# Kernel tuning notes

Hardware: AMD Instinct MI355X
Metric: run time of the kernel (lower is better)

The kernel has to match this reference:

```python
import jax, jax.numpy as jnp
import numpy as np

B, T, C = 8, 2048, 1024


def setup_inputs() -> dict:
    key = jax.random.key(0)
    ks = jax.random.split(key, 7)
    s = 0.02  # typical init scale for weights
    return {
        "x": jax.random.normal(ks[0], (B, T, C), jnp.float32),
        "wq": jax.random.normal(ks[1], (C, C), jnp.float32) * s,
        "bq": jax.random.normal(ks[2], (C,), jnp.float32) * s,
        "wk": jax.random.normal(ks[3], (C, C), jnp.float32) * s,
        "bk": jax.random.normal(ks[4], (C,), jnp.float32) * s,
        "wv": jax.random.normal(ks[5], (C, C), jnp.float32) * s,
        "bv": jax.random.normal(ks[6], (C,), jnp.float32) * s,
    }


def reference(x, wq, bq, wk, bk, wv, bv):
    # x: [B, T, C]; torch Linear stores weight as [out, in] -> x @ W.T + b
    Bx, Tx, Cx = x.shape
    Q = x @ wq.T + bq  # [B, T, C]
    K = x @ wk.T + bk
    V = x @ wv.T + bv
    # NOTE: source computes K @ Q^T (keys index rows, queries index columns)
    scores = jnp.einsum("btc,bsc->bts", K, Q) / jnp.sqrt(jnp.float32(Cx))  # [B, T, T]
    causal = jnp.tril(jnp.ones((Tx, Tx), dtype=bool))  # mask==0 above diagonal
    scores = jnp.where(causal, scores, -jnp.inf)
    # torch masked_fill with a (1,1,T,T) mask broadcasts scores to (1,B,T,T)
    scores = scores[None]  # [1, B, T, T]
    w = jax.nn.softmax(scores, axis=-1)
    out = jnp.einsum("abts,bsc->abtc", w, V)  # [1, B, T, C]
    return out
```

## Files before the change

kernel.cpp:

```cpp
#include <hip/hip_runtime.h>
#include <stdint.h>

typedef unsigned short u16;
typedef __attribute__((ext_vector_type(8))) __bf16 bf16x8;
typedef __attribute__((ext_vector_type(4))) float f32x4;

#define DEVI __device__ __forceinline__

DEVI u16 f32_to_bf16(float f) {
  uint32_t u = __builtin_bit_cast(uint32_t, f);
  u += 0x7FFFu + ((u >> 16) & 1u);
  return (u16)(u >> 16);
}

DEVI void gl2lds16(const void* g, void* l) {
  __builtin_amdgcn_global_load_lds(
      (const __attribute__((address_space(1))) void*)g,
      (__attribute__((address_space(3))) void*)l, 16, 0, 0);
}

#define S_BATCH 2228224

__global__ void cast_all_kernel(const float* __restrict__ x,
                                const float* __restrict__ wq,
                                const float* __restrict__ wk,
                                const float* __restrict__ wv,
                                u16* __restrict__ xb, u16* __restrict__ wb,
                                float* __restrict__ sums) {
  const int i0 = blockIdx.x * blockDim.x + threadIdx.x;
  const int stride = gridDim.x * blockDim.x;
  for (int j = i0; j < 4194304; j += stride) {
    const float4 v = ((const float4*)x)[j];
    ushort4 o;
    o.x = f32_to_bf16(v.x);
    o.y = f32_to_bf16(v.y);
    o.z = f32_to_bf16(v.z);
    o.w = f32_to_bf16(v.w);
    ((ushort4*)xb)[j] = o;
  }
  for (int j = i0; j < 786432; j += stride) {
    const int z = j >> 18;
    const int r = j & 262143;
    const float* src = (z == 0) ? wq : (z == 1) ? wk : wv;
    const float4 v = ((const float4*)src)[r];
    ushort4 o;
    o.x = f32_to_bf16(v.x);
    o.y = f32_to_bf16(v.y);
    o.z = f32_to_bf16(v.z);
    o.w = f32_to_bf16(v.w);
    ((ushort4*)(wb + (size_t)z * 1048576))[r] = o;
  }
  if (i0 < 4096) ((float4*)sums)[i0] = (float4){0.f, 0.f, 0.f, 0.f};
}

__global__ __launch_bounds__(512, 2) void qkv_kernel(
    const u16* __restrict__ xb, const u16* __restrict__ wb,
    const float* __restrict__ bq, const float* __restrict__ bk,
    const float* __restrict__ bv, u16* __restrict__ Qb, u16* __restrict__ Kb,
    u16* __restrict__ Vt) {
  __shared__ __align__(16) u16 lds[65536];

  const int id = blockIdx.x;
  const int wg = (id & 7) * 96 + (id >> 3);
  const int g = wg >> 3, u = wg & 7;
  const int z = g >> 5;
  const int tp = g & 31;
  const int tmt = tp * 2 + (u >> 2);
  const int tct = u & 3;

  int m0, n0;
  const u16* Aptr;
  const u16* Bptr;
  if (z < 2) {
    m0 = tct * 256;
    n0 = tmt * 256;
    Aptr = wb + (size_t)z * 1048576 + (size_t)m0 * 1024;
    Bptr = xb + (size_t)n0 * 1024;
  } else {
    m0 = tmt * 256;
    n0 = tct * 256;
    Aptr = xb + (size_t)m0 * 1024;
    Bptr = wb + (size_t)2 * 1048576 + (size_t)n0 * 1024;
  }

  const int tid = threadIdx.x;
  const int srow = tid >> 3;
  const int sgrp = ((tid & 7) - srow) & 7;
  const u16* Ag = Aptr + (size_t)srow * 1024 + sgrp * 8;
  const u16* Bg = Bptr + (size_t)srow * 1024 + sgrp * 8;
  char* ldsDst = (char*)lds + tid * 16;

#define ST_A0(kt) do { const u16* s_ = Ag + (kt) * 64;           char* d_ = ldsDst + (((kt) & 1) * 65536);         gl2lds16(s_, d_); gl2lds16(s_ + 65536, d_ + 8192); } while (0)
#define ST_A1(kt) do { const u16* s_ = Ag + 131072 + (kt) * 64;  char* d_ = ldsDst + (((kt) & 1) * 65536) + 16384; gl2lds16(s_, d_); gl2lds16(s_ + 65536, d_ + 8192); } while (0)
#define ST_B0(kt) do { const u16* s_ = Bg + (kt) * 64;           char* d_ = ldsDst + (((kt) & 1) * 65536) + 32768; gl2lds16(s_, d_); gl2lds16(s_ + 65536, d_ + 8192); } while (0)
#define ST_B1(kt) do { const u16* s_ = Bg + 131072 + (kt) * 64;  char* d_ = ldsDst + (((kt) & 1) * 65536) + 49152; gl2lds16(s_, d_); gl2lds16(s_ + 65536, d_ + 8192); } while (0)

  ST_A0(0); ST_B0(0); ST_B1(0); ST_A1(0);
  ST_A0(1); ST_B0(1); ST_B1(1);

  const int lane = tid & 63, wid = tid >> 6;
  const int wr = wid >> 2, wc = wid & 3;
  const int l15 = lane & 15, quad = lane >> 4;

  int aoff[4][2], boff[2][2];
#pragma unroll
  for (int i_ = 0; i_ < 4; ++i_) {
    const int arow = wr * 64 + i_ * 16 + l15;
#pragma unroll
    for (int k_ = 0; k_ < 2; ++k_)
      aoff[i_][k_] = arow * 64 + ((k_ * 4 + quad + arow) & 7) * 8;
  }
#pragma unroll
  for (int j_ = 0; j_ < 2; ++j_) {
    const int brow = wc * 32 + j_ * 16 + l15;
#pragma unroll
    for (int k_ = 0; k_ < 2; ++k_)
      boff[j_][k_] = brow * 64 + ((k_ * 4 + quad + brow) & 7) * 8;
  }

  f32x4 acc[2][2][4][2];
#pragma unroll
  for (int a_ = 0; a_ < 2; ++a_)
#pragma unroll
    for (int b_ = 0; b_ < 2; ++b_)
#pragma unroll
      for (int i_ = 0; i_ < 4; ++i_)
#pragma unroll
        for (int j_ = 0; j_ < 2; ++j_)
          acc[a_][b_][i_][j_] = (f32x4){0.f, 0.f, 0.f, 0.f};

  bf16x8 af[4][2], bfr[2][2][2];

#define LOADA(qm, buf) do { const u16* p_ = lds + (buf) * 32768 + (qm) * 8192; \
  _Pragma("unroll") for (int i_ = 0; i_ < 4; ++i_) \
  _Pragma("unroll") for (int k_ = 0; k_ < 2; ++k_) \
    af[i_][k_] = *(const bf16x8*)(p_ + aoff[i_][k_]); } while (0)
#define LOADB(qn, buf) do { const u16* p_ = lds + (buf) * 32768 + 16384 + (qn) * 8192; \
  _Pragma("unroll") for (int j_ = 0; j_ < 2; ++j_) \
  _Pragma("unroll") for (int k_ = 0; k_ < 2; ++k_) \
    bfr[qn][j_][k_] = *(const bf16x8*)(p_ + boff[j_][k_]); } while (0)
#define MMA(qm, qn) do { \
  _Pragma("unroll") for (int i_ = 0; i_ < 4; ++i_) \
  _Pragma("unroll") for (int j_ = 0; j_ < 2; ++j_) \
  _Pragma("unroll") for (int k_ = 0; k_ < 2; ++k_) \
    acc[qm][qn][i_][j_] = __builtin_amdgcn_mfma_f32_16x16x32_bf16( \
        af[i_][k_], bfr[qn][j_][k_], acc[qm][qn][i_][j_], 0, 0, 0); } while (0)

#define BAR __builtin_amdgcn_s_barrier()
#define WLG0 asm volatile("s_waitcnt lgkmcnt(0)")
#define WLG8 asm volatile("s_waitcnt lgkmcnt(8)")
#define PRIO1 __builtin_amdgcn_s_setprio(1)
#define PRIO0 __builtin_amdgcn_s_setprio(0)
#define WVM6 asm volatile("s_waitcnt vmcnt(6)" ::: "memory")
#define WVM0 asm volatile("s_waitcnt vmcnt(0)" ::: "memory")

  WVM6;
  BAR;

#pragma unroll 1
  for (int it = 0; it < 7; ++it) {
    const int j0 = 2 * it;
    LOADA(0, 0); LOADB(0, 0); ST_A1(j0 + 1); WLG8;
    BAR; WLG0; PRIO1; MMA(0, 0); PRIO0; BAR;
    LOADB(1, 0); ST_A0(j0 + 2);
    BAR; WLG0; PRIO1; MMA(0, 1); PRIO0; BAR;
    LOADA(1, 0); ST_B0(j0 + 2);
    BAR; WLG0; PRIO1; MMA(1, 1); PRIO0; BAR;
    ST_B1(j0 + 2);
    BAR; PRIO1; MMA(1, 0); PRIO0;
    WVM6;
    BAR;
    LOADA(0, 1); LOADB(0, 1); ST_A1(j0 + 2); WLG8;
    BAR; WLG0; PRIO1; MMA(0, 0); PRIO0; BAR;
    LOADB(1, 1); ST_A0(j0 + 3);
    BAR; WLG0; PRIO1; MMA(0, 1); PRIO0; BAR;
    LOADA(1, 1); ST_B0(j0 + 3);
    BAR; WLG0; PRIO1; MMA(1, 1); PRIO0; BAR;
    ST_B1(j0 + 3);
    BAR; PRIO1; MMA(1, 0); PRIO0;
    WVM6;
    BAR;
  }
  {
    LOADA(0, 0); LOADB(0, 0); ST_A1(15); WLG8;
    BAR; WLG0; PRIO1; MMA(0, 0); PRIO0; BAR;
    LOADB(1, 0);
    BAR; WLG0; PRIO1; MMA(0, 1); PRIO0; BAR;
    LOADA(1, 0);
    BAR; WLG0; PRIO1; MMA(1, 1); PRIO0; BAR;
    BAR; PRIO1; MMA(1, 0); PRIO0;
    WVM0;
    BAR;
    LOADA(0, 1); LOADB(0, 1); WLG8;
    BAR; WLG0; PRIO1; MMA(0, 0); PRIO0; BAR;
    LOADB(1, 1);
    BAR; WLG0; PRIO1; MMA(0, 1); PRIO0; BAR;
    LOADA(1, 1);
    BAR; WLG0; PRIO1; MMA(1, 1); PRIO0; BAR;
    PRIO1; MMA(1, 0); PRIO0;
    BAR;
  }

  if (z < 2) {
    const float* bias = (z == 0) ? bq : bk;
    u16* Out = (z == 0) ? Qb : Kb;
#pragma unroll
    for (int th = 0; th < 2; ++th) {
      if (th) __syncthreads();
#pragma unroll
      for (int qm = 0; qm < 2; ++qm)
#pragma unroll
        for (int i_ = 0; i_ < 4; ++i_) {
          const int c = qm * 128 + wr * 64 + i_ * 16 + quad * 4;
          const float4 b4 = *(const float4*)(bias + m0 + c);
#pragma unroll
          for (int j_ = 0; j_ < 2; ++j_) {
            const int row = wc * 32 + j_ * 16 + l15;
            ushort4 o;
            o.x = f32_to_bf16(acc[qm][th][i_][j_][0] + b4.x);
            o.y = f32_to_bf16(acc[qm][th][i_][j_][1] + b4.y);
            o.z = f32_to_bf16(acc[qm][th][i_][j_][2] + b4.z);
            o.w = f32_to_bf16(acc[qm][th][i_][j_][3] + b4.w);
            *(ushort4*)(lds + row * 264 + c) = o;
          }
        }
      __syncthreads();
#pragma unroll
      for (int p = 0; p < 8; ++p) {
        const int row = p * 16 + (tid >> 5);
        const int c0 = (tid & 31) * 8;
        const uint4 v = *(const uint4*)(lds + row * 264 + c0);
        *(uint4*)(Out + (size_t)(n0 + th * 128 + row) * 1024 + m0 + c0) = v;
      }
    }
  } else {
    const int b = m0 >> 11;
    const int t0b = m0 & 2047;
    u16* Out = Vt + (size_t)b * 2097152;
#pragma unroll
    for (int th = 0; th < 2; ++th) {
      if (th) __syncthreads();
#pragma unroll
      for (int j_ = 0; j_ < 2; ++j_) {
        const int row = wc * 32 + j_ * 16 + l15;
        const float bb = bv[n0 + th * 128 + row];
#pragma unroll
        for (int qm = 0; qm < 2; ++qm)
#pragma unroll
          for (int i_ = 0; i_ < 4; ++i_) {
            const int c = qm * 128 + wr * 64 + i_ * 16 + quad * 4;
            ushort4 o;
            o.x = f32_to_bf16(acc[qm][th][i_][j_][0] + bb);
            o.y = f32_to_bf16(acc[qm][th][i_][j_][1] + bb);
            o.z = f32_to_bf16(acc[qm][th][i_][j_][2] + bb);
            o.w = f32_to_bf16(acc[qm][th][i_][j_][3] + bb);
            *(ushort4*)(lds + row * 264 + c) = o;
          }
      }
      __syncthreads();
#pragma unroll
      for (int p = 0; p < 8; ++p) {
        const int row = p * 16 + (tid >> 5);
        const int c0 = (tid & 31) * 8;
        const uint4 v = *(const uint4*)(lds + row * 264 + c0);
        *(uint4*)(Out + (size_t)(n0 + th * 128 + row) * 2048 + t0b + c0) = v;
      }
    }
  }
#undef ST_A0
#undef ST_A1
#undef ST_B0
#undef ST_B1
#undef LOADA
#undef LOADB
#undef MMA
#undef BAR
#undef WLG0
#undef WLG8
#undef PRIO1
#undef PRIO0
#undef WVM6
#undef WVM0
}

__global__ __launch_bounds__(512, 2) void score_kernel(const u16* __restrict__ Kb,
                                                       const u16* __restrict__ Qb,
                                                       u16* __restrict__ Spk,
                                                       float* __restrict__ sums) {
  __shared__ __align__(16) u16 lds[49152];

  const int id = blockIdx.x;
  const int b = id & 7;
  const int l = id >> 3;
  int k = (int)((sqrtf(4.f * l + 1.f) - 1.f) * 0.5f);
  if (k * (k + 1) > l) --k;
  if ((k + 1) * (k + 2) <= l) ++k;
  const int off = l - k * (k + 1);
  const int hi = (off >= (k + 1));
  const int rt = 2 * k + hi;
  const int ct = off - (hi ? (k + 1) : 0);
  const bool maskT = (ct == k);

  const int tid = threadIdx.x;
  const int srow = tid >> 3;
  const int sgrp = ((tid & 7) - srow) & 7;
  const u16* A = Qb + ((size_t)b * 2048 + ct * 256) * 1024;
  const u16* B = Kb + ((size_t)b * 2048 + rt * 128) * 1024;
  const u16* Ag = A + (size_t)srow * 1024 + sgrp * 8;
  const u16* Bg = B + (size_t)srow * 1024 + sgrp * 8;
  char* ldsDst = (char*)lds + tid * 16;

#define ST_A0(kt) do { const u16* s_ = Ag + (kt) * 64;           char* d_ = ldsDst + (((kt) & 1) * 49152);         gl2lds16(s_, d_); gl2lds16(s_ + 65536, d_ + 8192); } while (0)
#define ST_A1(kt) do { const u16* s_ = Ag + 131072 + (kt) * 64;  char* d_ = ldsDst + (((kt) & 1) * 49152) + 16384; gl2lds16(s_, d_); gl2lds16(s_ + 65536, d_ + 8192); } while (0)
#define ST_B(kt)  do { const u16* s_ = Bg + (kt) * 64;           char* d_ = ldsDst + (((kt) & 1) * 49152) + 32768; gl2lds16(s_, d_); gl2lds16(s_ + 65536, d_ + 8192); } while (0)

  ST_A0(0); ST_B(0); ST_A1(0);
  ST_A0(1); ST_B(1);

  const int lane = tid & 63, wid = tid >> 6;
  const int wr = wid >> 2, wc = wid & 3;
  const int l15 = lane & 15, quad = lane >> 4;

  int aoff[4][2], boff[2][2];
#pragma unroll
  for (int i_ = 0; i_ < 4; ++i_) {
    const int arow = wr * 64 + i_ * 16 + l15;
#pragma unroll
    for (int k_ = 0; k_ < 2; ++k_)
      aoff[i_][k_] = arow * 64 + ((k_ * 4 + quad + arow) & 7) * 8;
  }
#pragma unroll
  for (int j_ = 0; j_ < 2; ++j_) {
    const int brow = wc * 32 + j_ * 16 + l15;
#pragma unroll
    for (int k_ = 0; k_ < 2; ++k_)
      boff[j_][k_] = brow * 64 + ((k_ * 4 + quad + brow) & 7) * 8;
  }

  f32x4 acc[2][4][2];
#pragma unroll
  for (int q_ = 0; q_ < 2; ++q_)
#pragma unroll
    for (int i_ = 0; i_ < 4; ++i_)
#pragma unroll
      for (int j_ = 0; j_ < 2; ++j_)
        acc[q_][i_][j_] = (f32x4){0.f, 0.f, 0.f, 0.f};

  bf16x8 af[4][2], bfr[2][2];

#define SLOADA(qm, buf) do { const u16* p_ = lds + (buf) * 24576 + (qm) * 8192; \
  _Pragma("unroll") for (int i_ = 0; i_ < 4; ++i_) \
  _Pragma("unroll") for (int k_ = 0; k_ < 2; ++k_) \
    af[i_][k_] = *(const bf16x8*)(p_ + aoff[i_][k_]); } while (0)
#define SLOADB(buf) do { const u16* p_ = lds + (buf) * 24576 + 16384; \
  _Pragma("unroll") for (int j_ = 0; j_ < 2; ++j_) \
  _Pragma("unroll") for (int k_ = 0; k_ < 2; ++k_) \
    bfr[j_][k_] = *(const bf16x8*)(p_ + boff[j_][k_]); } while (0)
#define SMMA(qm) do { \
  _Pragma("unroll") for (int i_ = 0; i_ < 4; ++i_) \
  _Pragma("unroll") for (int j_ = 0; j_ < 2; ++j_) \
  _Pragma("unroll") for (int k_ = 0; k_ < 2; ++k_) \
    acc[qm][i_][j_] = __builtin_amdgcn_mfma_f32_16x16x32_bf16( \
        af[i_][k_], bfr[j_][k_], acc[qm][i_][j_], 0, 0, 0); } while (0)

#define BAR __builtin_amdgcn_s_barrier()
#define WLG0 asm volatile("s_waitcnt lgkmcnt(0)")
#define PRIO1 __builtin_amdgcn_s_setprio(1)
#define PRIO0 __builtin_amdgcn_s_setprio(0)
#define WVM4 asm volatile("s_waitcnt vmcnt(4)" ::: "memory")
#define WVM0 asm volatile("s_waitcnt vmcnt(0)" ::: "memory")

  WVM4;
  BAR;

#pragma unroll 1
  for (int it = 0; it < 7; ++it) {
    const int j0 = 2 * it;
    SLOADA(0, 0); SLOADB(0); ST_A1(j0 + 1);
    BAR; WLG0; PRIO1; SMMA(0); PRIO0; BAR;
    SLOADA(1, 0); ST_A0(j0 + 2); ST_B(j0 + 2);
    BAR; WLG0; PRIO1; SMMA(1); PRIO0;
    WVM4;
    BAR;
    SLOADA(0, 1); SLOADB(1); ST_A1(j0 + 2);
    BAR; WLG0; PRIO1; SMMA(0); PRIO0; BAR;
    SLOADA(1, 1); ST_A0(j0 + 3); ST_B(j0 + 3);
    BAR; WLG0; PRIO1; SMMA(1); PRIO0;
    WVM4;
    BAR;
  }
  {
    SLOADA(0, 0); SLOADB(0); ST_A1(15);
    BAR; WLG0; PRIO1; SMMA(0); PRIO0; BAR;
    SLOADA(1, 0);
    BAR; WLG0; PRIO1; SMMA(1); PRIO0;
    WVM0;
    BAR;
    SLOADA(0, 1); SLOADB(1);
    BAR; WLG0; PRIO1; SMMA(0); PRIO0; BAR;
    SLOADA(1, 1);
    BAR; WLG0; PRIO1; SMMA(1); PRIO0; BAR;
  }

  const int moff = (rt & 1) * 128;
  float sj[2] = {0.f, 0.f};
#pragma unroll
  for (int qm = 0; qm < 2; ++qm)
#pragma unroll
    for (int i_ = 0; i_ < 4; ++i_) {
      const int s0 = qm * 128 + wr * 64 + i_ * 16 + quad * 4;
#pragma unroll
      for (int j_ = 0; j_ < 2; ++j_) {
        const int t = wc * 32 + j_ * 16 + l15;
        ushort4 o;
        float e[4];
#pragma unroll
        for (int r = 0; r < 4; ++r) {
          float v = __expf(acc[qm][i_][j_][r] * 0.03125f);
          if (maskT && (s0 + r) > (t + moff)) v = 0.f;
          e[r] = v;
          sj[j_] += v;
        }
        o.x = f32_to_bf16(e[0]);
        o.y = f32_to_bf16(e[1]);
        o.z = f32_to_bf16(e[2]);
        o.w = f32_to_bf16(e[3]);
        *(ushort4*)(lds + t * 264 + s0) = o;
      }
    }
#pragma unroll
  for (int j_ = 0; j_ < 2; ++j_) {
    float v = sj[j_];
    v += __shfl_xor(v, 16);
    v += __shfl_xor(v, 32);
    if (quad == 0)
      atomicAdd(&sums[(size_t)b * 2048 + rt * 128 + wc * 32 + j_ * 16 + l15], v);
  }
  __syncthreads();
  const int ld = (rt + 1) * 128;
  const int nc = ld - ct * 256;
  u16* Out = Spk + (size_t)b * S_BATCH + (size_t)(rt * (rt + 1) / 2) * 16384 +
             ct * 256;
  if (nc >= 256) {
#pragma unroll
    for (int p = 0; p < 8; ++p) {
      const int row = p * 16 + (tid >> 5);
      const int c0 = (tid & 31) * 8;
      const uint4 v = *(const uint4*)(lds + row * 264 + c0);
      *(uint4*)(Out + (size_t)row * ld + c0) = v;
    }
  } else {
#pragma unroll
    for (int p = 0; p < 4; ++p) {
      const int row = p * 32 + (tid >> 4);
      const int c0 = (tid & 15) * 8;
      const uint4 v = *(const uint4*)(lds + row * 264 + c0);
      *(uint4*)(Out + (size_t)row * ld + c0) = v;
    }
  }
#undef ST_A0
#undef ST_A1
#undef ST_B
#undef SLOADA
#undef SLOADB
#undef SMMA
#undef BAR
#undef WLG0
#undef PRIO1
#undef PRIO0
#undef WVM4
#undef WVM0
}

__global__ __launch_bounds__(512, 2) void pv_kernel(const u16* __restrict__ Spk,
                                                    const u16* __restrict__ Vt,
                                                    const float* __restrict__ sums,
                                                    float* __restrict__ Out) {
  __shared__ __align__(16) u16 lds[49152];

  const int id = blockIdx.x;
  const int hf = id >> 8;
  const int rr_ = id & 255;
  const int rt = (hf ? 7 : 15) - (rr_ >> 5);
  const int ct = (rr_ >> 3) & 3;
  const int b = rr_ & 7;

  const int ldb = (rt + 1) * 128;
  const int nk2 = rt + 1;

  const int tid = threadIdx.x;
  const int srow = tid >> 3;
  const int sgrp = ((tid & 7) - srow) & 7;
  const u16* A = Vt + ((size_t)b * 1024 + ct * 256) * 2048;
  const u16* B = Spk + (size_t)b * S_BATCH +
                 (size_t)(rt * (rt + 1) / 2) * 16384;
  const u16* Ag = A + (size_t)srow * 2048 + sgrp * 8;
  const u16* Bg = B + (size_t)srow * ldb + sgrp * 8;
  char* ldsDst = (char*)lds + tid * 16;

#define ST_A0(kt) do { const u16* s_ = Ag + (kt) * 64;            char* d_ = ldsDst + (((kt) & 1) * 49152);         gl2lds16(s_, d_); gl2lds16(s_ + 131072, d_ + 8192); } while (0)
#define ST_A1(kt) do { const u16* s_ = Ag + 262144 + (kt) * 64;   char* d_ = ldsDst + (((kt) & 1) * 49152) + 16384; gl2lds16(s_, d_); gl2lds16(s_ + 131072, d_ + 8192); } while (0)
#define ST_B(kt)  do { const u16* s_ = Bg + (kt) * 64;            char* d_ = ldsDst + (((kt) & 1) * 49152) + 32768; gl2lds16(s_, d_); gl2lds16(s_ + (size_t)64 * ldb, d_ + 8192); } while (0)

  ST_A0(0); ST_B(0); ST_A1(0);
  ST_A0(1); ST_B(1);

  const int lane = tid & 63, wid = tid >> 6;
  const int wr = wid >> 2, wc = wid & 3;
  const int l15 = lane & 15, quad = lane >> 4;

  int aoff[4][2], boff[2][2];
#pragma unroll
  for (int i_ = 0; i_ < 4; ++i_) {
    const int arow = wr * 64 + i_ * 16 + l15;
#pragma unroll
    for (int k_ = 0; k_ < 2; ++k_)
      aoff[i_][k_] = arow * 64 + ((k_ * 4 + quad + arow) & 7) * 8;
  }
#pragma unroll
  for (int j_ = 0; j_ < 2; ++j_) {
    const int brow = wc * 32 + j_ * 16 + l15;
#pragma unroll
    for (int k_ = 0; k_ < 2; ++k_)
      boff[j_][k_] = brow * 64 + ((k_ * 4 + quad + brow) & 7) * 8;
  }

  f32x4 acc[2][4][2];
#pragma unroll
  for (int q_ = 0; q_ < 2; ++q_)
#pragma unroll
    for (int i_ = 0; i_ < 4; ++i_)
#pragma unroll
      for (int j_ = 0; j_ < 2; ++j_)
        acc[q_][i_][j_] = (f32x4){0.f, 0.f, 0.f, 0.f};

  bf16x8 af[4][2], bfr[2][2];

#define SLOADA(qm, buf) do { const u16* p_ = lds + (buf) * 24576 + (qm) * 8192; \
  _Pragma("unroll") for (int i_ = 0; i_ < 4; ++i_) \
  _Pragma("unroll") for (int k_ = 0; k_ < 2; ++k_) \
    af[i_][k_] = *(const bf16x8*)(p_ + aoff[i_][k_]); } while (0)
#define SLOADB(buf) do { const u16* p_ = lds + (buf) * 24576 + 16384; \
  _Pragma("unroll") for (int j_ = 0; j_ < 2; ++j_) \
  _Pragma("unroll") for (int k_ = 0; k_ < 2; ++k_) \
    bfr[j_][k_] = *(const bf16x8*)(p_ + boff[j_][k_]); } while (0)
#define SMMA(qm) do { \
  _Pragma("unroll") for (int i_ = 0; i_ < 4; ++i_) \
  _Pragma("unroll") for (int j_ = 0; j_ < 2; ++j_) \
  _Pragma("unroll") for (int k_ = 0; k_ < 2; ++k_) \
    acc[qm][i_][j_] = __builtin_amdgcn_mfma_f32_16x16x32_bf16( \
        af[i_][k_], bfr[j_][k_], acc[qm][i_][j_], 0, 0, 0); } while (0)

#define BAR __builtin_amdgcn_s_barrier()
#define WLG0 asm volatile("s_waitcnt lgkmcnt(0)")
#define PRIO1 __builtin_amdgcn_s_setprio(1)
#define PRIO0 __builtin_amdgcn_s_setprio(0)
#define WVM4 asm volatile("s_waitcnt vmcnt(4)" ::: "memory")
#define WVM0 asm volatile("s_waitcnt vmcnt(0)" ::: "memory")

  WVM4;
  BAR;

#pragma unroll 1
  for (int it = 0; it < nk2 - 1; ++it) {
    const int j0 = 2 * it;
    SLOADA(0, 0); SLOADB(0); ST_A1(j0 + 1);
    BAR; WLG0; PRIO1; SMMA(0); PRIO0; BAR;
    SLOADA(1, 0); ST_A0(j0 + 2); ST_B(j0 + 2);
    BAR; WLG0; PRIO1; SMMA(1); PRIO0;
    WVM4;
    BAR;
    SLOADA(0, 1); SLOADB(1); ST_A1(j0 + 2);
    BAR; WLG0; PRIO1; SMMA(0); PRIO0; BAR;
    SLOADA(1, 1); ST_A0(j0 + 3); ST_B(j0 + 3);
    BAR; WLG0; PRIO1; SMMA(1); PRIO0;
    WVM4;
    BAR;
  }
  {
    SLOADA(0, 0); SLOADB(0); ST_A1(2 * nk2 - 1);
    BAR; WLG0; PRIO1; SMMA(0); PRIO0; BAR;
    SLOADA(1, 0);
    BAR; WLG0; PRIO1; SMMA(1); PRIO0;
    WVM0;
    BAR;
    SLOADA(0, 1); SLOADB(1);
    BAR; WLG0; PRIO1; SMMA(0); PRIO0; BAR;
    SLOADA(1, 1);
    BAR; WLG0; PRIO1; SMMA(1); PRIO0; BAR;
  }

  float* ftile = (float*)lds;
  const float* sumsb = sums + (size_t)b * 2048 + rt * 128;
  float* Ob = Out + (size_t)b * 2048 * 1024 + (size_t)(rt * 128) * 1024 +
              ct * 256;
  float iv[2];
#pragma unroll
  for (int j_ = 0; j_ < 2; ++j_)
    iv[j_] = 1.0f / sumsb[wc * 32 + j_ * 16 + l15];
#pragma unroll
  for (int qm = 0; qm < 2; ++qm) {
    if (qm) __syncthreads();
#pragma unroll
    for (int i_ = 0; i_ < 4; ++i_) {
      const int c0 = wr * 64 + i_ * 16 + quad * 4;
#pragma unroll
      for (int j_ = 0; j_ < 2; ++j_) {
        const int t = wc * 32 + j_ * 16 + l15;
        float4 v;
        v.x = acc[qm][i_][j_][0] * iv[j_];
        v.y = acc[qm][i_][j_][1] * iv[j_];
        v.z = acc[qm][i_][j_][2] * iv[j_];
        v.w = acc[qm][i_][j_][3] * iv[j_];
        *(float4*)(ftile + t * 132 + c0) = v;
      }
    }
    __syncthreads();
#pragma unroll
    for (int p = 0; p < 8; ++p) {
      const int row = p * 16 + (tid >> 5);
      const int c0f = (tid & 31) * 4;
      const float4 v = *(const float4*)(ftile + row * 132 + c0f);
      *(float4*)(Ob + (size_t)row * 1024 + qm * 128 + c0f) = v;
    }
  }
#undef ST_A0
#undef ST_A1
#undef ST_B
#undef SLOADA
#undef SLOADB
#undef SMMA
#undef BAR
#undef WLG0
#undef PRIO1
#undef PRIO0
#undef WVM4
#undef WVM0
}

extern "C" void kernel_launch(void* const* d_in, const int* in_sizes, int n_in,
                              void* d_out, int out_size, void* d_ws,
                              size_t ws_size, hipStream_t stream) {
  const float* x = (const float*)d_in[0];
  const float* wq = (const float*)d_in[1];
  const float* bq = (const float*)d_in[2];
  const float* wk = (const float*)d_in[3];
  const float* bk = (const float*)d_in[4];
  const float* wv = (const float*)d_in[5];
  const float* bv = (const float*)d_in[6];
  float* out = (float*)d_out;
  char* ws = (char*)d_ws;

  u16* Qb = (u16*)(ws);
  u16* Kb = (u16*)(ws + ((size_t)32 << 20));
  u16* Vt = (u16*)(ws + ((size_t)64 << 20));
  u16* Spk = (u16*)(ws + ((size_t)96 << 20));
  u16* xb = (u16*)(ws + ((size_t)96 << 20));
  float* sums = (float*)(ws + ((size_t)132 << 20));
  u16* wb = (u16*)(ws + ((size_t)134 << 20));

  cast_all_kernel<<<2048, 256, 0, stream>>>(x, wq, wk, wv, xb, wb, sums);

  qkv_kernel<<<768, 512, 0, stream>>>(xb, wb, bq, bk, bv, Qb, Kb, Vt);

  score_kernel<<<576, 512, 0, stream>>>(Kb, Qb, Spk, sums);

  pv_kernel<<<512, 512, 0, stream>>>(Spk, Vt, sums, out);
}
```

Before: 324.9 us.

## Retile score kernel to 128x192 tiles with smaller LDS and higher occupancy

The score kernel's Q-side tile shrinks from 256 to 192 columns, and LDS per block drops from 96KB to 80KB. Launch bounds now request 4 blocks per CU, and the grid grows from 576 to 768 blocks via a new per-row tile count. The goal is better triangular-workload balance, less wasted work on diagonal tiles, and more resident blocks to hide latency. In exchange there is less reuse per loaded K tile, a deeper six-phase pipeline with more barriers, a serial loop to decode the tile index, and a causal mask check applied on every tile.

```diff
diff --git a/kernel.cpp b/kernel.cpp
--- a/kernel.cpp
+++ b/kernel.cpp
@@ -283,51 +283,54 @@
 #undef WVM0
 }
 
-__global__ __launch_bounds__(512, 2) void score_kernel(const u16* __restrict__ Kb,
+__global__ __launch_bounds__(512, 4) void score_kernel(const u16* __restrict__ Kb,
                                                        const u16* __restrict__ Qb,
                                                        u16* __restrict__ Spk,
                                                        float* __restrict__ sums) {
-  __shared__ __align__(16) u16 lds[49152];
+  __shared__ __align__(16) u16 lds[40960];
 
   const int id = blockIdx.x;
   const int b = id & 7;
-  const int l = id >> 3;
-  int k = (int)((sqrtf(4.f * l + 1.f) - 1.f) * 0.5f);
-  if (k * (k + 1) > l) --k;
-  if ((k + 1) * (k + 2) <= l) ++k;
-  const int off = l - k * (k + 1);
-  const int hi = (off >= (k + 1));
-  const int rt = 2 * k + hi;
-  const int ct = off - (hi ? (k + 1) : 0);
-  const bool maskT = (ct == k);
+  int rem = id >> 3;
+  int rt = 0;
+  for (;;) {
+    const int n = (2 * rt + 4) / 3;
+    if (rem < n) break;
+    rem -= n;
+    ++rt;
+  }
+  const int ct = rem;
+  const int sbase = ct * 192;
+  const int tbase = rt * 128;
 
   const int tid = threadIdx.x;
   const int srow = tid >> 3;
   const int sgrp = ((tid & 7) - srow) & 7;
-  const u16* A = Qb + ((size_t)b * 2048 + ct * 256) * 1024;
-  const u16* B = Kb + ((size_t)b * 2048 + rt * 128) * 1024;
+  const u16* A = Qb + ((size_t)b * 2048 + sbase) * 1024;
+  const u16* B = Kb + ((size_t)b * 2048 + tbase) * 1024;
   const u16* Ag = A + (size_t)srow * 1024 + sgrp * 8;
   const u16* Bg = B + (size_t)srow * 1024 + sgrp * 8;
   char* ldsDst = (char*)lds + tid * 16;
 
-#define ST_A0(kt) do { const u16* s_ = Ag + (kt) * 64;           char* d_ = ldsDst + (((kt) & 1) * 49152);         gl2lds16(s_, d_); gl2lds16(s_ + 65536, d_ + 8192); } while (0)
-#define ST_A1(kt) do { const u16* s_ = Ag + 131072 + (kt) * 64;  char* d_ = ldsDst + (((kt) & 1) * 49152) + 16384; gl2lds16(s_, d_); gl2lds16(s_ + 65536, d_ + 8192); } while (0)
-#define ST_B(kt)  do { const u16* s_ = Bg + (kt) * 64;           char* d_ = ldsDst + (((kt) & 1) * 49152) + 32768; gl2lds16(s_, d_); gl2lds16(s_ + 65536, d_ + 8192); } while (0)
-
-  ST_A0(0); ST_B(0); ST_A1(0);
-  ST_A0(1); ST_B(1);
+#define ST_A0(kt) gl2lds16(Ag + (kt) * 64,           ldsDst + ((kt) & 1) * 40960)
+#define ST_A1(kt) gl2lds16(Ag + 65536 + (kt) * 64,   ldsDst + ((kt) & 1) * 40960 + 8192)
+#define ST_A2(kt) gl2lds16(Ag + 131072 + (kt) * 64,  ldsDst + ((kt) & 1) * 40960 + 16384)
+#define ST_B(kt)  do { const u16* s_ = Bg + (kt) * 64; char* d_ = ldsDst + ((kt) & 1) * 40960 + 24576; gl2lds16(s_, d_); gl2lds16(s_ + 65536, d_ + 8192); } while (0)
+
+  ST_A0(0); ST_B(0); ST_A1(0); ST_A2(0);
+  ST_A0(1); ST_B(1); ST_A1(1);
 
   const int lane = tid & 63, wid = tid >> 6;
   const int wr = wid >> 2, wc = wid & 3;
   const int l15 = lane & 15, quad = lane >> 4;
 
-  int aoff[4][2], boff[2][2];
-#pragma unroll
-  for (int i_ = 0; i_ < 4; ++i_) {
-    const int arow = wr * 64 + i_ * 16 + l15;
+  int aoff[2][2], boff[2][2];
+#pragma unroll
+  for (int i_ = 0; i_ < 2; ++i_) {
+    const int ar = wr * 32 + i_ * 16 + l15;
 #pragma unroll
     for (int k_ = 0; k_ < 2; ++k_)
-      aoff[i_][k_] = arow * 64 + ((k_ * 4 + quad + arow) & 7) * 8;
+      aoff[i_][k_] = ar * 64 + ((k_ * 4 + quad + ar) & 7) * 8;
   }
 #pragma unroll
   for (int j_ = 0; j_ < 2; ++j_) {
@@ -337,78 +340,78 @@
       boff[j_][k_] = brow * 64 + ((k_ * 4 + quad + brow) & 7) * 8;
   }
 
-  f32x4 acc[2][4][2];
-#pragma unroll
-  for (int q_ = 0; q_ < 2; ++q_)
-#pragma unroll
-    for (int i_ = 0; i_ < 4; ++i_)
+  f32x4 acc[3][2][2];
+#pragma unroll
+  for (int p_ = 0; p_ < 3; ++p_)
+#pragma unroll
+    for (int i_ = 0; i_ < 2; ++i_)
 #pragma unroll
       for (int j_ = 0; j_ < 2; ++j_)
-        acc[q_][i_][j_] = (f32x4){0.f, 0.f, 0.f, 0.f};
-
-  bf16x8 af[4][2], bfr[2][2];
-
-#define SLOADA(qm, buf) do { const u16* p_ = lds + (buf) * 24576 + (qm) * 8192; \
-  _Pragma("unroll") for (int i_ = 0; i_ < 4; ++i_) \
+        acc[p_][i_][j_] = (f32x4){0.f, 0.f, 0.f, 0.f};
+
+  bf16x8 af[2][2], bfr[2][2];
+
+#define SLA(p, buf) do { const u16* p_ = lds + (buf) * 20480 + (p) * 4096; \
+  _Pragma("unroll") for (int i_ = 0; i_ < 2; ++i_) \
   _Pragma("unroll") for (int k_ = 0; k_ < 2; ++k_) \
     af[i_][k_] = *(const bf16x8*)(p_ + aoff[i_][k_]); } while (0)
-#define SLOADB(buf) do { const u16* p_ = lds + (buf) * 24576 + 16384; \
+#define SLB(buf) do { const u16* p_ = lds + (buf) * 20480 + 12288; \
   _Pragma("unroll") for (int j_ = 0; j_ < 2; ++j_) \
   _Pragma("unroll") for (int k_ = 0; k_ < 2; ++k_) \
     bfr[j_][k_] = *(const bf16x8*)(p_ + boff[j_][k_]); } while (0)
-#define SMMA(qm) do { \
-  _Pragma("unroll") for (int i_ = 0; i_ < 4; ++i_) \
+#define SMMA(p) do { \
+  _Pragma("unroll") for (int i_ = 0; i_ < 2; ++i_) \
   _Pragma("unroll") for (int j_ = 0; j_ < 2; ++j_) \
   _Pragma("unroll") for (int k_ = 0; k_ < 2; ++k_) \
-    acc[qm][i_][j_] = __builtin_amdgcn_mfma_f32_16x16x32_bf16( \
-        af[i_][k_], bfr[j_][k_], acc[qm][i_][j_], 0, 0, 0); } while (0)
+    acc[p][i_][j_] = __builtin_amdgcn_mfma_f32_16x16x32_bf16( \
+        af[i_][k_], bfr[j_][k_], acc[p][i_][j_], 0, 0, 0); } while (0)
 
 #define BAR __builtin_amdgcn_s_barrier()
 #define WLG0 asm volatile("s_waitcnt lgkmcnt(0)")
 #define PRIO1 __builtin_amdgcn_s_setprio(1)
 #define PRIO0 __builtin_amdgcn_s_setprio(0)
-#define WVM4 asm volatile("s_waitcnt vmcnt(4)" ::: "memory")
-#define WVM0 asm volatile("s_waitcnt vmcnt(0)" ::: "memory")
-
-  WVM4;
+#define WVM(n) asm volatile("s_waitcnt vmcnt(" #n ")" ::: "memory")
+
+  WVM(6);
   BAR;
 
 #pragma unroll 1
   for (int it = 0; it < 7; ++it) {
     const int j0 = 2 * it;
-    SLOADA(0, 0); SLOADB(0); ST_A1(j0 + 1);
-    BAR; WLG0; PRIO1; SMMA(0); PRIO0; BAR;
-    SLOADA(1, 0); ST_A0(j0 + 2); ST_B(j0 + 2);
-    BAR; WLG0; PRIO1; SMMA(1); PRIO0;
-    WVM4;
-    BAR;
-    SLOADA(0, 1); SLOADB(1); ST_A1(j0 + 2);
-    BAR; WLG0; PRIO1; SMMA(0); PRIO0; BAR;
-    SLOADA(1, 1); ST_A0(j0 + 3); ST_B(j0 + 3);
-    BAR; WLG0; PRIO1; SMMA(1); PRIO0;
-    WVM4;
-    BAR;
+    SLA(0, 0); SLB(0); ST_A2(j0 + 1);
+    BAR; WLG0; PRIO1; SMMA(0); PRIO0; WVM(6); BAR;
+    SLA(1, 0); ST_A0(j0 + 2); ST_B(j0 + 2);
+    BAR; WLG0; PRIO1; SMMA(1); PRIO0; WVM(8); BAR;
+    SLA(2, 0); ST_A1(j0 + 2);
+    BAR; WLG0; PRIO1; SMMA(2); PRIO0; WVM(6); BAR;
+    SLA(0, 1); SLB(1); ST_A2(j0 + 2);
+    BAR; WLG0; PRIO1; SMMA(0); PRIO0; WVM(6); BAR;
+    SLA(1, 1); ST_A0(j0 + 3); ST_B(j0 + 3);
+    BAR; WLG0; PRIO1; SMMA(1); PRIO0; WVM(8); BAR;
+    SLA(2, 1); ST_A1(j0 + 3);
+    BAR; WLG0; PRIO1; SMMA(2); PRIO0; WVM(6); BAR;
   }
   {
-    SLOADA(0, 0); SLOADB(0); ST_A1(15);
-    BAR; WLG0; PRIO1; SMMA(0); PRIO0; BAR;
-    SLOADA(1, 0);
-    BAR; WLG0; PRIO1; SMMA(1); PRIO0;
-    WVM0;
-    BAR;
-    SLOADA(0, 1); SLOADB(1);
-    BAR; WLG0; PRIO1; SMMA(0); PRIO0; BAR;
-    SLOADA(1, 1);
-    BAR; WLG0; PRIO1; SMMA(1); PRIO0; BAR;
-  }
-
-  const int moff = (rt & 1) * 128;
+    SLA(0, 0); SLB(0); ST_A2(15);
+    BAR; WLG0; PRIO1; SMMA(0); PRIO0; WVM(6); BAR;
+    SLA(1, 0);
+    BAR; WLG0; PRIO1; SMMA(1); PRIO0; WVM(5); BAR;
+    SLA(2, 0);
+    BAR; WLG0; PRIO1; SMMA(2); PRIO0; WVM(2); BAR;
+    SLA(0, 1); SLB(1);
+    BAR; WLG0; PRIO1; SMMA(0); PRIO0; WVM(1); BAR;
+    SLA(1, 1);
+    BAR; WLG0; PRIO1; SMMA(1); PRIO0; WVM(0); BAR;
+    SLA(2, 1);
+    BAR; WLG0; PRIO1; SMMA(2); PRIO0; BAR;
+  }
+
   float sj[2] = {0.f, 0.f};
 #pragma unroll
-  for (int qm = 0; qm < 2; ++qm)
-#pragma unroll
-    for (int i_ = 0; i_ < 4; ++i_) {
-      const int s0 = qm * 128 + wr * 64 + i_ * 16 + quad * 4;
+  for (int p_ = 0; p_ < 3; ++p_)
+#pragma unroll
+    for (int i_ = 0; i_ < 2; ++i_) {
+      const int s0 = p_ * 64 + wr * 32 + i_ * 16 + quad * 4;
 #pragma unroll
       for (int j_ = 0; j_ < 2; ++j_) {
         const int t = wc * 32 + j_ * 16 + l15;
@@ -416,8 +419,8 @@
         float e[4];
 #pragma unroll
         for (int r = 0; r < 4; ++r) {
-          float v = __expf(acc[qm][i_][j_][r] * 0.03125f);
-          if (maskT && (s0 + r) > (t + moff)) v = 0.f;
+          float v = __expf(acc[p_][i_][j_][r] * 0.03125f);
+          if ((sbase + s0 + r) > (tbase + t)) v = 0.f;
           e[r] = v;
           sj[j_] += v;
         }
@@ -425,7 +428,7 @@
         o.y = f32_to_bf16(e[1]);
         o.z = f32_to_bf16(e[2]);
         o.w = f32_to_bf16(e[3]);
-        *(ushort4*)(lds + t * 264 + s0) = o;
+        *(ushort4*)(lds + t * 200 + s0) = o;
       }
     }
 #pragma unroll
@@ -434,42 +437,37 @@
     v += __shfl_xor(v, 16);
     v += __shfl_xor(v, 32);
     if (quad == 0)
-      atomicAdd(&sums[(size_t)b * 2048 + rt * 128 + wc * 32 + j_ * 16 + l15], v);
+      atomicAdd(&sums[(size_t)b * 2048 + tbase + wc * 32 + j_ * 16 + l15], v);
   }
   __syncthreads();
   const int ld = (rt + 1) * 128;
-  const int nc = ld - ct * 256;
+  const int nc = (ld - sbase < 192) ? (ld - sbase) : 192;
   u16* Out = Spk + (size_t)b * S_BATCH + (size_t)(rt * (rt + 1) / 2) * 16384 +
-             ct * 256;
-  if (nc >= 256) {
-#pragma unroll
-    for (int p = 0; p < 8; ++p) {
-      const int row = p * 16 + (tid >> 5);
-      const int c0 = (tid & 31) * 8;
-      const uint4 v = *(const uint4*)(lds + row * 264 + c0);
-      *(uint4*)(Out + (size_t)row * ld + c0) = v;
-    }
-  } else {
-#pragma unroll
-    for (int p = 0; p < 4; ++p) {
-      const int row = p * 32 + (tid >> 4);
-      const int c0 = (tid & 15) * 8;
-      const uint4 v = *(const uint4*)(lds + row * 264 + c0);
-      *(uint4*)(Out + (size_t)row * ld + c0) = v;
+             sbase;
+#pragma unroll
+  for (int cp = 0; cp < 3; ++cp) {
+    if (cp * 64 < nc) {
+#pragma unroll
+      for (int h = 0; h < 2; ++h) {
+        const int row = h * 64 + (tid >> 3);
+        const int c0 = cp * 64 + (tid & 7) * 8;
+        const uint4 v = *(const uint4*)(lds + row * 200 + c0);
+        *(uint4*)(Out + (size_t)row * ld + c0) = v;
+      }
     }
   }
 #undef ST_A0
 #undef ST_A1
+#undef ST_A2
 #undef ST_B
-#undef SLOADA
-#undef SLOADB
+#undef SLA
+#undef SLB
 #undef SMMA
 #undef BAR
 #undef WLG0
 #undef PRIO1
 #undef PRIO0
-#undef WVM4
-#undef WVM0
+#undef WVM
 }
 
 __global__ __launch_bounds__(512, 2) void pv_kernel(const u16* __restrict__ Spk,
@@ -663,7 +661,7 @@
 
   qkv_kernel<<<768, 512, 0, stream>>>(xb, wb, bq, bk, bv, Qb, Kb, Vt);
 
-  score_kernel<<<576, 512, 0, stream>>>(Kb, Qb, Spk, sums);
+  score_kernel<<<768, 512, 0, stream>>>(Kb, Qb, Spk, sums);
 
   pv_kernel<<<512, 512, 0, stream>>>(Spk, Vt, sums, out);
 }
```

After: 300.8 us. 7.4% less time.
